# Performance work log

Hardware: AMD Instinct MI355X
Metric: run time of the kernel (lower is better)

Reference implementation:

```python
import jax, jax.numpy as jnp
import numpy as np

D = 1024
H = 16
DH = D // H  # 64
EPS = 1e-5


def _ln(x, w, b=None):
    mu = jnp.mean(x, axis=-1, keepdims=True)
    var = jnp.var(x, axis=-1, keepdims=True)
    y = (x - mu) * jax.lax.rsqrt(var + EPS) * w
    return y + b if b is not None else y


def _rotate_half(x):
    x1, x2 = jnp.split(x, 2, axis=-1)
    return jnp.concatenate([-x2, x1], axis=-1)


def _rope(q, k):
    # q, k: [B, L, H, DH]; rotary over sequence dim (ESM-style half-split rotation)
    L = q.shape[1]
    inv_freq = 1.0 / (10000.0 ** (jnp.arange(0, DH, 2, dtype=jnp.float32) / DH))
    freqs = jnp.arange(L, dtype=jnp.float32)[:, None] * inv_freq[None, :]  # [L, DH/2]
    emb = jnp.concatenate([freqs, freqs], axis=-1)  # [L, DH]
    cos = jnp.cos(emb)[None, :, None, :]  # [1, L, 1, DH]
    sin = jnp.sin(emb)[None, :, None, :]
    q = q * cos + _rotate_half(q) * sin
    k = k * cos + _rotate_half(k) * sin
    return q, k


def setup_inputs() -> dict:
    key = jax.random.key(0)
    ks = jax.random.split(key, 8)
    B, L = 2, 2048
    x = jax.random.normal(ks[0], (B, L, D), dtype=jnp.float32)
    seq_id = jnp.sort(jax.random.randint(ks[1], (B, L), 0, 8), axis=-1)
    s = 1.0 / np.sqrt(D)
    return {
        "x": x,
        "seq_id": seq_id,
        "ln1_w": jnp.ones((D,), jnp.float32),
        "ln1_b": jnp.zeros((D,), jnp.float32),
        "w_qkv": jax.random.normal(ks[2], (3 * D, D), dtype=jnp.float32) * s,
        "q_ln_w": jnp.ones((D,), jnp.float32),
        "k_ln_w": jnp.ones((D,), jnp.float32),
        "out_w": jax.random.normal(ks[3], (D, D), dtype=jnp.float32) * s,
    }


def reference(x, seq_id, ln1_w, ln1_b, w_qkv, q_ln_w, k_ln_w, out_w):
    B, L, _ = x.shape
    h = _ln(x, ln1_w, ln1_b)
    qkv = jnp.einsum("bld,ed->ble", h, w_qkv)  # [B, L, 3D]
    q, k, v = jnp.split(qkv, 3, axis=-1)
    q = _ln(q, q_ln_w)
    k = _ln(k, k_ln_w)
    q = q.reshape(B, L, H, DH)
    k = k.reshape(B, L, H, DH)
    q, k = _rope(q, k)
    q = q.transpose(0, 2, 1, 3)  # [B, H, L, DH]
    k = k.transpose(0, 2, 1, 3)
    v = v.reshape(B, L, H, DH).transpose(0, 2, 1, 3)
    scale = 1.0 / np.sqrt(DH)
    scores = jnp.einsum("bhld,bhmd->bhlm", q, k) * scale  # [B, H, L, L]
    mask = (seq_id[:, None, :, None] == seq_id[:, None, None, :])  # [B, 1, L, L]
    scores = jnp.where(mask, scores, -jnp.inf)
    attn = jax.nn.softmax(scores, axis=-1)
    ctx = jnp.einsum("bhlm,bhmd->bhld", attn, v)  # [B, H, L, DH]
    ctx = ctx.transpose(0, 2, 1, 3).reshape(B, L, D)
    return jnp.einsum("bld,ed->ble", ctx, out_w)
```

## Files before the change

kernel.cpp:

```cpp
#include <hip/hip_runtime.h>
#include <hip/hip_bf16.h>
#include <math.h>

#define D 1024
#define H 16
#define DH 64
#define L 2048
#define B 2
#define NROW (B * L)
#define EPS 1e-5f

typedef _Float16 half8 __attribute__((ext_vector_type(8)));
typedef _Float16 half4v __attribute__((ext_vector_type(4)));
typedef float f32x4 __attribute__((ext_vector_type(4)));

__global__ __launch_bounds__(256) void prep_kernel(const float* __restrict__ x,
                                                   const float* __restrict__ lw,
                                                   const float* __restrict__ lb,
                                                   _Float16* __restrict__ h16,
                                                   const float* __restrict__ wqkv,
                                                   _Float16* __restrict__ wqkv16,
                                                   const float* __restrict__ outw,
                                                   _Float16* __restrict__ outw16,
                                                   const int* __restrict__ seq_id,
                                                   int* __restrict__ lo,
                                                   int* __restrict__ hi,
                                                   float2* __restrict__ rtab) {
    int blk = blockIdx.x;
    int t = threadIdx.x;
    if (blk < 4096) {
        int r = blk;
        const float* xr = x + (size_t)r * D;
        float4 v = *(const float4*)&xr[t * 4];
        float s = v.x + v.y + v.z + v.w;
        float sq = v.x * v.x + v.y * v.y + v.z * v.z + v.w * v.w;
        for (int off = 32; off > 0; off >>= 1) {
            s += __shfl_xor(s, off, 64);
            sq += __shfl_xor(sq, off, 64);
        }
        __shared__ float ls[4], lq[4];
        int wave = t >> 6;
        if ((t & 63) == 0) { ls[wave] = s; lq[wave] = sq; }
        __syncthreads();
        float S = ls[0] + ls[1] + ls[2] + ls[3];
        float Q = lq[0] + lq[1] + lq[2] + lq[3];
        float mu = S / (float)D;
        float rs = rsqrtf(Q / (float)D - mu * mu + EPS);
        float4 w4 = *(const float4*)&lw[t * 4];
        float4 b4 = *(const float4*)&lb[t * 4];
        half4v o = {(_Float16)((v.x - mu) * rs * w4.x + b4.x),
                    (_Float16)((v.y - mu) * rs * w4.y + b4.y),
                    (_Float16)((v.z - mu) * rs * w4.z + b4.z),
                    (_Float16)((v.w - mu) * rs * w4.w + b4.w)};
        *(half4v*)&h16[(size_t)r * D + t * 4] = o;
    } else if (blk < 6144) {
        int base = blk - 4096;
        const float* src;
        _Float16* dst;
        if (base < 1536) { src = wqkv; dst = wqkv16; }
        else             { src = outw; dst = outw16; base -= 1536; }
        int i = (base * 256 + t) * 8;
        float4 a = *(const float4*)&src[i];
        float4 b = *(const float4*)&src[i + 4];
        half8 h = {(_Float16)a.x, (_Float16)a.y, (_Float16)a.z, (_Float16)a.w,
                   (_Float16)b.x, (_Float16)b.y, (_Float16)b.z, (_Float16)b.w};
        *(half8*)&dst[i] = h;
    } else if (blk < 6160) {
        int idx = (blk - 6144) * 256 + t;
        int b = idx / L, l = idx - b * L;
        const int* row = seq_id + (size_t)b * L;
        int v = row[l];
        int a = 0, c = L;
        while (a < c) { int m = (a + c) >> 1; if (row[m] < v) a = m + 1; else c = m; }
        lo[idx] = a;
        a = 0; c = L;
        while (a < c) { int m = (a + c) >> 1; if (row[m] <= v) a = m + 1; else c = m; }
        hi[idx] = a;
    } else {
        int idx = (blk - 6160) * 256 + t;
        int l = idx >> 5, fi = idx & 31;
        float invf = expf(-(float)fi * 0.28782313662425572f);
        float sn, cs;
        sincosf((float)l * invf, &sn, &cs);
        rtab[idx] = make_float2(cs, sn);
    }
}

template <typename OutT, int BM, int BN, bool VSPLIT>
__global__ __launch_bounds__(256) void gemm_f16_kernel(const _Float16* __restrict__ A,
                                                       const _Float16* __restrict__ W,
                                                       OutT* __restrict__ C, int N,
                                                       _Float16* __restrict__ v_t) {
    constexpr int WM = BM / 2, WN = BN / 2;
    constexpr int MT = WM / 16, NT = WN / 16;
    __shared__ _Float16 As[2][BM * 32];
    __shared__ _Float16 Bs[2][BN * 32];
    int t = threadIdx.x;
    int w = t >> 6, lane = t & 63;
    int quad = lane >> 4, col = lane & 15;
    int nx = gridDim.x;
    int ib = blockIdx.y * nx + blockIdx.x;
    int nwg = nx * gridDim.y;
    int ni = (ib & 7) * (nwg >> 3) + (ib >> 3);
    int m0 = (ni / nx) * BM, n0 = (ni % nx) * BN;
    int mw = (w >> 1) * WM, nw = (w & 1) * WN;
    int sw = (col >> 1) & 3;

    f32x4 acc[MT][NT] = {};

    auto stage = [&](int k0, int buf) {
#pragma unroll
        for (int i = 0; i < BM / 64; i++) {
            int e = t + i * 256;
            int row = e >> 2, kc = (e & 3) ^ ((row >> 1) & 3);
            __builtin_amdgcn_global_load_lds(
                (const __attribute__((address_space(1))) void*)&A[(size_t)(m0 + row) * 1024 + k0 + kc * 8],
                (__attribute__((address_space(3))) void*)&As[buf][e * 8], 16, 0, 0);
        }
#pragma unroll
        for (int i = 0; i < BN / 64; i++) {
            int e = t + i * 256;
            int row = e >> 2, kc = (e & 3) ^ ((row >> 1) & 3);
            __builtin_amdgcn_global_load_lds(
                (const __attribute__((address_space(1))) void*)&W[(size_t)(n0 + row) * 1024 + k0 + kc * 8],
                (__attribute__((address_space(3))) void*)&Bs[buf][e * 8], 16, 0, 0);
        }
    };

    stage(0, 0);
    int cur = 0;
    for (int k0 = 0; k0 < 1024; k0 += 32) {
        __syncthreads();
        if (k0 + 32 < 1024) stage(k0 + 32, cur ^ 1);
        half8 af[MT], bf[NT];
#pragma unroll
        for (int mt = 0; mt < MT; mt++)
            af[mt] = *(const half8*)&As[cur][(mw + mt * 16 + col) * 32 + ((quad ^ sw) << 3)];
#pragma unroll
        for (int nt = 0; nt < NT; nt++)
            bf[nt] = *(const half8*)&Bs[cur][(nw + nt * 16 + col) * 32 + ((quad ^ sw) << 3)];
#pragma unroll
        for (int mt = 0; mt < MT; mt++)
#pragma unroll
            for (int nt = 0; nt < NT; nt++)
                acc[mt][nt] = __builtin_amdgcn_mfma_f32_16x16x32_f16(af[mt], bf[nt], acc[mt][nt], 0, 0, 0);
        cur ^= 1;
    }

    if (VSPLIT && n0 >= 2048) {
        int b = m0 >> 11;
#pragma unroll
        for (int mt = 0; mt < MT; mt++)
#pragma unroll
            for (int nt = 0; nt < NT; nt++) {
                int vcol = n0 - 2048 + nw + nt * 16 + col;
                int bh = b * H + (vcol >> 6);
                int d = vcol & 63;
                int l = (m0 & (L - 1)) + mw + mt * 16 + quad * 4;
                half4v pk = {(_Float16)acc[mt][nt][0], (_Float16)acc[mt][nt][1],
                             (_Float16)acc[mt][nt][2], (_Float16)acc[mt][nt][3]};
                *(half4v*)&v_t[((size_t)(bh * 64 + d)) * 2048 + l] = pk;
            }
    } else {
#pragma unroll
        for (int mt = 0; mt < MT; mt++)
#pragma unroll
            for (int nt = 0; nt < NT; nt++)
#pragma unroll
                for (int r = 0; r < 4; r++) {
                    int row = m0 + mw + mt * 16 + quad * 4 + r;
                    int cc = n0 + nw + nt * 16 + col;
                    C[(size_t)row * N + cc] = (OutT)acc[mt][nt][r];
                }
    }
}

__global__ __launch_bounds__(256) void mid_kernel(const _Float16* __restrict__ qkv,
                                                  const float* __restrict__ qw,
                                                  const float* __restrict__ kw,
                                                  const float2* __restrict__ rtab,
                                                  _Float16* __restrict__ q_r,
                                                  _Float16* __restrict__ k_r) {
    __shared__ float ls[4], lq[4];
    int t = threadIdx.x;
    int r = blockIdx.x;
    int half = t >> 7;
    int tt = t & 127;
    const _Float16* src = qkv + (size_t)r * 3072 + half * 1024;
    const float* wgt = half ? kw : qw;
    _Float16* dst = half ? k_r : q_r;

    half8 hv = *(const half8*)&src[tt * 8];
    float y[8];
    float s = 0.f, sq = 0.f;
#pragma unroll
    for (int e = 0; e < 8; e++) {
        float v = (float)hv[e];
        y[e] = v;
        s += v;
        sq += v * v;
    }
    for (int off = 32; off > 0; off >>= 1) {
        s += __shfl_xor(s, off, 64);
        sq += __shfl_xor(sq, off, 64);
    }
    int wave = t >> 6;
    if ((t & 63) == 0) { ls[wave] = s; lq[wave] = sq; }
    __syncthreads();
    int base = half << 1;
    float S = ls[base] + ls[base + 1];
    float Q = lq[base] + lq[base + 1];
    float mu = S / 1024.f;
    float rs = rsqrtf(Q / 1024.f - mu * mu + EPS);

    int l = r & (L - 1);
    int b = r >> 11;
    int j0 = tt * 8;
    int dh0 = j0 & 63, hh = j0 >> 6;
    const float2* cp = &rtab[l * 32 + (dh0 & 31)];
    float4 c01 = *(const float4*)cp;
    float4 c23 = *(const float4*)(cp + 2);
    float4 c45 = *(const float4*)(cp + 4);
    float4 c67 = *(const float4*)(cp + 6);
    float cs_[8] = {c01.x, c01.z, c23.x, c23.z, c45.x, c45.z, c67.x, c67.z};
    float sn_[8] = {c01.y, c01.w, c23.y, c23.w, c45.y, c45.w, c67.y, c67.w};

    float yn[8];
#pragma unroll
    for (int e = 0; e < 8; e++) yn[e] = (y[e] - mu) * rs * wgt[j0 + e];
    float sgn = (dh0 < 32) ? -1.f : 1.f;
    half8 o;
#pragma unroll
    for (int e = 0; e < 8; e++) {
        float p = __shfl_xor(yn[e], 4, 64);
        o[e] = (_Float16)(yn[e] * cs_[e] + sgn * p * sn_[e]);
    }
    *(half8*)&dst[((size_t)((b * H + hh) * L + l)) * 64 + dh0] = o;
}

__global__ __launch_bounds__(512) void attn_mfma_kernel(const _Float16* __restrict__ q_r,
                                                        const _Float16* __restrict__ k_r,
                                                        const _Float16* __restrict__ v_t,
                                                        const int* __restrict__ lo_arr,
                                                        const int* __restrict__ hi_arr,
                                                        _Float16* __restrict__ ctx) {
    __shared__ _Float16 Ks[2][64][64];
    __shared__ _Float16 Vs[2][64][64];
    __shared__ _Float16 Ps[8][16][64];
    int bh = blockIdx.y;
    int b = bh >> 4, h = bh & 15;
    int l0 = blockIdx.x * 128;
    int t = threadIdx.x;
    int w = t >> 6, lane = t & 63;
    int quad = lane >> 4, col = lane & 15;
    int rbase = l0 + w * 16;

    int blo = lo_arr[b * L + l0] & ~63;
    int bhi = hi_arr[b * L + l0 + 127];

    auto stage = [&](int m0, int buf) {
        int row = t >> 3, ch = t & 7;
        int sch = ch ^ (row & 7);
        __builtin_amdgcn_global_load_lds(
            (const __attribute__((address_space(1))) void*)&k_r[((size_t)(bh * L + m0 + row)) * 64 + sch * 8],
            (__attribute__((address_space(3))) void*)&Ks[buf][row][ch * 8], 16, 0, 0);
        __builtin_amdgcn_global_load_lds(
            (const __attribute__((address_space(1))) void*)&v_t[((size_t)(bh * 64 + row)) * 2048 + m0 + sch * 8],
            (__attribute__((address_space(3))) void*)&Vs[buf][row][ch * 8], 16, 0, 0);
    };

    stage(blo, 0);

    half8 qf0, qf1;
    {
        const _Float16* qp = q_r + ((size_t)(bh * L + rbase + col)) * 64 + quad * 8;
        qf0 = *(const half8*)qp;
        qf1 = *(const half8*)(qp + 32);
    }
    int lo_c = lo_arr[b * L + rbase + col];
    int hi_c = hi_arr[b * L + rbase + col];
    int wlo = __shfl(lo_c, 15, 64);
    int whi = __shfl(hi_c, 0, 64);

    f32x4 o[4] = {};
    float m_run = -1e30f, l_run = 0.f;
    const float SCL = 0.125f * 1.4426950408889634f;
    int swz = (col & 7) << 3;
    int src = (lane & 48) | ((lane & 48) >> 2);

    int cur = 0;
    for (int m0 = blo; m0 < bhi; m0 += 64) {
        __syncthreads();
        if (m0 + 64 < bhi) stage(m0 + 64, cur ^ 1);

        f32x4 s[4] = {};
#pragma unroll
        for (int nt = 0; nt < 4; nt++) {
            int key = nt * 16 + col;
            const _Float16* kp = &Ks[cur][key][0];
            half8 kf0 = *(const half8*)&kp[(quad ^ (key & 7)) * 8];
            half8 kf1 = *(const half8*)&kp[((quad + 4) ^ (key & 7)) * 8];
            s[nt] = __builtin_amdgcn_mfma_f32_16x16x32_f16(kf0, qf0, s[nt], 0, 0, 0);
            s[nt] = __builtin_amdgcn_mfma_f32_16x16x32_f16(kf1, qf1, s[nt], 0, 0, 0);
        }

        float p[4][4];
        bool full = (m0 >= wlo) && (m0 + 64 <= whi);
        if (full) {
#pragma unroll
            for (int nt = 0; nt < 4; nt++)
#pragma unroll
                for (int r = 0; r < 4; r++) p[nt][r] = s[nt][r] * SCL;
        } else {
#pragma unroll
            for (int nt = 0; nt < 4; nt++) {
                int kb = m0 + nt * 16 + quad * 4;
#pragma unroll
                for (int r = 0; r < 4; r++) {
                    int key = kb + r;
                    p[nt][r] = (key >= lo_c && key < hi_c) ? s[nt][r] * SCL : -INFINITY;
                }
            }
        }

        float tmax = p[0][0];
#pragma unroll
        for (int nt = 0; nt < 4; nt++)
#pragma unroll
            for (int r = 0; r < 4; r++) tmax = fmaxf(tmax, p[nt][r]);
        tmax = fmaxf(tmax, __shfl_xor(tmax, 16, 64));
        tmax = fmaxf(tmax, __shfl_xor(tmax, 32, 64));
        float nm = fmaxf(m_run, tmax);
        float corr = exp2f(m_run - nm);
        m_run = nm;
        float rs = 0.f;
#pragma unroll
        for (int nt = 0; nt < 4; nt++)
#pragma unroll
            for (int r = 0; r < 4; r++) {
                float e2 = exp2f(p[nt][r] - nm);
                p[nt][r] = e2;
                rs += e2;
            }
        rs += __shfl_xor(rs, 16, 64);
        rs += __shfl_xor(rs, 32, 64);
        l_run = l_run * corr + rs;

#pragma unroll
        for (int nt = 0; nt < 4; nt++) {
            half4v pk = {(_Float16)p[nt][0], (_Float16)p[nt][1],
                         (_Float16)p[nt][2], (_Float16)p[nt][3]};
            *(half4v*)&Ps[w][col][(nt * 16 + quad * 4) ^ swz] = pk;
        }

#pragma unroll
        for (int r = 0; r < 4; r++) {
            float c4 = __shfl(corr, src + r, 64);
            o[0][r] *= c4; o[1][r] *= c4; o[2][r] *= c4; o[3][r] *= c4;
        }

        half8 pf0 = *(const half8*)&Ps[w][col][(quad * 8) ^ swz];
        half8 pf1 = *(const half8*)&Ps[w][col][(32 + quad * 8) ^ swz];
#pragma unroll
        for (int nt = 0; nt < 4; nt++) {
            int dr = nt * 16 + col;
            const _Float16* vp = &Vs[cur][dr][0];
            half8 vf0 = *(const half8*)&vp[(quad ^ (dr & 7)) * 8];
            half8 vf1 = *(const half8*)&vp[((quad + 4) ^ (dr & 7)) * 8];
            o[nt] = __builtin_amdgcn_mfma_f32_16x16x32_f16(pf0, vf0, o[nt], 0, 0, 0);
            o[nt] = __builtin_amdgcn_mfma_f32_16x16x32_f16(pf1, vf1, o[nt], 0, 0, 0);
        }
        cur ^= 1;
    }

#pragma unroll
    for (int r = 0; r < 4; r++) {
        float linv = 1.f / __shfl(l_run, src + r, 64);
        int row = rbase + quad * 4 + r;
#pragma unroll
        for (int nt = 0; nt < 4; nt++)
            ctx[((size_t)(b * L + row)) * 1024 + h * 64 + nt * 16 + col] =
                (_Float16)(o[nt][r] * linv);
    }
}

extern "C" void kernel_launch(void* const* d_in, const int* in_sizes, int n_in,
                              void* d_out, int out_size, void* d_ws, size_t ws_size,
                              hipStream_t stream) {
    const float* x      = (const float*)d_in[0];
    const int*   seq_id = (const int*)d_in[1];
    const float* ln1_w  = (const float*)d_in[2];
    const float* ln1_b  = (const float*)d_in[3];
    const float* w_qkv  = (const float*)d_in[4];
    const float* q_ln_w = (const float*)d_in[5];
    const float* k_ln_w = (const float*)d_in[6];
    const float* out_w  = (const float*)d_in[7];
    float* out = (float*)d_out;

    char* ws = (char*)d_ws;
    int*      lo     = (int*)(ws);
    int*      hi     = (int*)(ws + (64 << 10));
    float2*   rtab   = (float2*)(ws + (128 << 10));
    _Float16* h16    = (_Float16*)(ws + (1ull << 20));
    _Float16* wqkv16 = (_Float16*)(ws + (10ull << 20));
    _Float16* outw16 = (_Float16*)(ws + (17ull << 20));
    _Float16* qkv16  = (_Float16*)(ws + (20ull << 20));
    _Float16* q_r    = (_Float16*)(ws + (45ull << 20));
    _Float16* k_r    = (_Float16*)(ws + (54ull << 20));
    _Float16* v_t    = (_Float16*)(ws + (63ull << 20));
    _Float16* ctx16  = (_Float16*)(ws + (72ull << 20));

    prep_kernel<<<dim3(6416), dim3(256), 0, stream>>>(
        x, ln1_w, ln1_b, h16, w_qkv, wqkv16, out_w, outw16, seq_id, lo, hi, rtab);
    gemm_f16_kernel<_Float16, 128, 128, true><<<dim3(3072 / 128, NROW / 128), dim3(256), 0, stream>>>(
        h16, wqkv16, qkv16, 3072, v_t);
    mid_kernel<<<dim3(4096), dim3(256), 0, stream>>>(qkv16, q_ln_w, k_ln_w, rtab, q_r, k_r);
    attn_mfma_kernel<<<dim3(L / 128, B * H), dim3(512), 0, stream>>>(q_r, k_r, v_t, lo, hi, ctx16);
    gemm_f16_kernel<float, 128, 64, false><<<dim3(1024 / 64, NROW / 128), dim3(256), 0, stream>>>(
        ctx16, outw16, out, 1024, nullptr);

    (void)in_sizes; (void)n_in; (void)out_size; (void)ws_size;
}
```

Measured before the change: 186.0 us.

## Replace QKV GEMM with 256x256 eight-phase pipelined kernel using direct-to-LDS loads

Adds a dedicated QKV projection kernel with 256x256 tiles, 512 threads and a K-step of 64. It loads global data straight into XOR-swizzled LDS with global_load_lds. Each K iteration is split into four load/MMA phases with barriers and setprio, so the next tile's loads overlap with MFMA work. A CU-aware tile remap covers 192 blocks. The goal is higher MFMA utilization and operand reuse in the largest GEMM. The costs are more register pressure, more barriers, and a grid smaller than the CU count, which can leave some CUs idle.

```diff
diff --git a/kernel.cpp b/kernel.cpp
--- a/kernel.cpp
+++ b/kernel.cpp
@@ -86,11 +86,140 @@
     }
 }
 
-template <typename OutT, int BM, int BN, bool VSPLIT>
+#define LDA_HALF(BUF, MH, DST)                                                      \
+    _Pragma("unroll") for (int mt = 0; mt < 4; mt++) {                              \
+        int row_ = mw + (MH) * 64 + mt * 16 + col;                                  \
+        _Pragma("unroll") for (int kk = 0; kk < 2; kk++)                            \
+            DST[mt][kk] = *(const half8*)&As[BUF][row_][((kk * 4 + quad) ^ (row_ & 7)) * 8]; \
+    }
+
+#define LDB_HALF(BUF, NH, DST)                                                      \
+    _Pragma("unroll") for (int nt = 0; nt < 2; nt++) {                              \
+        int row_ = nw + (NH) * 32 + nt * 16 + col;                                  \
+        _Pragma("unroll") for (int kk = 0; kk < 2; kk++)                            \
+            DST[nt][kk] = *(const half8*)&Bs[BUF][row_][((kk * 4 + quad) ^ (row_ & 7)) * 8]; \
+    }
+
+#define MMA_QUAD(MH, NH, AF, BF)                                                    \
+    __builtin_amdgcn_s_setprio(1);                                                  \
+    _Pragma("unroll") for (int mt = 0; mt < 4; mt++)                                \
+    _Pragma("unroll") for (int nt = 0; nt < 2; nt++) {                              \
+        acc[(MH) * 4 + mt][(NH) * 2 + nt] = __builtin_amdgcn_mfma_f32_16x16x32_f16( \
+            AF[mt][0], BF[nt][0], acc[(MH) * 4 + mt][(NH) * 2 + nt], 0, 0, 0);      \
+        acc[(MH) * 4 + mt][(NH) * 2 + nt] = __builtin_amdgcn_mfma_f32_16x16x32_f16( \
+            AF[mt][1], BF[nt][1], acc[(MH) * 4 + mt][(NH) * 2 + nt], 0, 0, 0);      \
+    }                                                                               \
+    __builtin_amdgcn_s_setprio(0);
+
+__global__ __launch_bounds__(512, 2) void gemm1_8phase(const _Float16* __restrict__ A,
+                                                       const _Float16* __restrict__ W,
+                                                       _Float16* __restrict__ C,
+                                                       _Float16* __restrict__ v_t) {
+    __shared__ _Float16 As[2][256][64];
+    __shared__ _Float16 Bs[2][256][64];
+    int t = threadIdx.x;
+    int w = t >> 6, lane = t & 63;
+    int quad = lane >> 4, col = lane & 15;
+
+    int i = blockIdx.y * 12 + blockIdx.x;
+    int xcd = i & 7, j = i >> 3;
+    int tm = (xcd >> 1) * 4 + j / 6;
+    int tn = (xcd & 1) * 6 + j % 6;
+    int m0 = tm * 256, n0 = tn * 256;
+    int mw = (w >> 2) * 128, nw = (w & 3) * 64;
+
+    f32x4 acc[8][4] = {};
+
+    auto stageA = [&](int kt, int buf, int half) {
+#pragma unroll
+        for (int ii = 0; ii < 2; ii++) {
+            int e = half * 1024 + ii * 512 + t;
+            int row = e >> 3, ch = e & 7;
+            int sch = ch ^ (row & 7);
+            __builtin_amdgcn_global_load_lds(
+                (const __attribute__((address_space(1))) void*)&A[(size_t)(m0 + row) * 1024 + kt * 64 + sch * 8],
+                (__attribute__((address_space(3))) void*)&As[buf][row][ch * 8], 16, 0, 0);
+        }
+    };
+    auto stageB = [&](int kt, int buf, int half) {
+#pragma unroll
+        for (int ii = 0; ii < 2; ii++) {
+            int e = half * 1024 + ii * 512 + t;
+            int row = e >> 3, ch = e & 7;
+            int sch = ch ^ (row & 7);
+            __builtin_amdgcn_global_load_lds(
+                (const __attribute__((address_space(1))) void*)&W[(size_t)(n0 + row) * 1024 + kt * 64 + sch * 8],
+                (__attribute__((address_space(3))) void*)&Bs[buf][row][ch * 8], 16, 0, 0);
+        }
+    };
+
+    stageA(0, 0, 0); stageA(0, 0, 1); stageB(0, 0, 0); stageB(0, 0, 1);
+    stageA(1, 1, 0);
+    asm volatile("s_waitcnt vmcnt(2)" ::: "memory");
+    __builtin_amdgcn_s_barrier();
+
+    half8 af[4][2], bf0[2][2], bf1[2][2];
+    for (int kt = 0; kt < 16; kt++) {
+        int p = kt & 1, np = p ^ 1;
+
+        LDA_HALF(p, 0, af);
+        LDB_HALF(p, 0, bf0);
+        if (kt + 1 < 16) stageA(kt + 1, np, 1);
+        __builtin_amdgcn_s_barrier();
+        MMA_QUAD(0, 0, af, bf0);
+        __builtin_amdgcn_s_barrier();
+
+        LDB_HALF(p, 1, bf1);
+        if (kt + 1 < 16) stageB(kt + 1, np, 0);
+        __builtin_amdgcn_s_barrier();
+        MMA_QUAD(0, 1, af, bf1);
+        __builtin_amdgcn_s_barrier();
+
+        LDA_HALF(p, 1, af);
+        if (kt + 1 < 16) stageB(kt + 1, np, 1);
+        __builtin_amdgcn_s_barrier();
+        MMA_QUAD(1, 1, af, bf1);
+        __builtin_amdgcn_s_barrier();
+
+        if (kt + 2 < 16) stageA(kt + 2, p, 0);
+        MMA_QUAD(1, 0, af, bf0);
+        if (kt < 14)       { asm volatile("s_waitcnt vmcnt(2)" ::: "memory"); }
+        else if (kt == 14) { asm volatile("s_waitcnt vmcnt(0)" ::: "memory"); }
+        if (kt < 15) __builtin_amdgcn_s_barrier();
+    }
+
+    if (n0 >= 2048) {
+        int b = m0 >> 11;
+#pragma unroll
+        for (int mt = 0; mt < 8; mt++)
+#pragma unroll
+            for (int nt = 0; nt < 4; nt++) {
+                int vcol = n0 - 2048 + nw + nt * 16 + col;
+                int bh = b * H + (vcol >> 6);
+                int d = vcol & 63;
+                int l = (m0 & (L - 1)) + mw + mt * 16 + quad * 4;
+                half4v pk = {(_Float16)acc[mt][nt][0], (_Float16)acc[mt][nt][1],
+                             (_Float16)acc[mt][nt][2], (_Float16)acc[mt][nt][3]};
+                *(half4v*)&v_t[((size_t)(bh * 64 + d)) * 2048 + l] = pk;
+            }
+    } else {
+#pragma unroll
+        for (int mt = 0; mt < 8; mt++)
+#pragma unroll
+            for (int nt = 0; nt < 4; nt++)
+#pragma unroll
+                for (int r = 0; r < 4; r++) {
+                    int row = m0 + mw + mt * 16 + quad * 4 + r;
+                    int cc = n0 + nw + nt * 16 + col;
+                    C[(size_t)row * 3072 + cc] = (_Float16)acc[mt][nt][r];
+                }
+    }
+}
+
+template <typename OutT, int BM, int BN>
 __global__ __launch_bounds__(256) void gemm_f16_kernel(const _Float16* __restrict__ A,
                                                        const _Float16* __restrict__ W,
-                                                       OutT* __restrict__ C, int N,
-                                                       _Float16* __restrict__ v_t) {
+                                                       OutT* __restrict__ C, int N) {
     constexpr int WM = BM / 2, WN = BN / 2;
     constexpr int MT = WM / 16, NT = WN / 16;
     __shared__ _Float16 As[2][BM * 32];
@@ -147,32 +276,16 @@
         cur ^= 1;
     }
 
-    if (VSPLIT && n0 >= 2048) {
-        int b = m0 >> 11;
-#pragma unroll
-        for (int mt = 0; mt < MT; mt++)
-#pragma unroll
-            for (int nt = 0; nt < NT; nt++) {
-                int vcol = n0 - 2048 + nw + nt * 16 + col;
-                int bh = b * H + (vcol >> 6);
-                int d = vcol & 63;
-                int l = (m0 & (L - 1)) + mw + mt * 16 + quad * 4;
-                half4v pk = {(_Float16)acc[mt][nt][0], (_Float16)acc[mt][nt][1],
-                             (_Float16)acc[mt][nt][2], (_Float16)acc[mt][nt][3]};
-                *(half4v*)&v_t[((size_t)(bh * 64 + d)) * 2048 + l] = pk;
+#pragma unroll
+    for (int mt = 0; mt < MT; mt++)
+#pragma unroll
+        for (int nt = 0; nt < NT; nt++)
+#pragma unroll
+            for (int r = 0; r < 4; r++) {
+                int row = m0 + mw + mt * 16 + quad * 4 + r;
+                int cc = n0 + nw + nt * 16 + col;
+                C[(size_t)row * N + cc] = (OutT)acc[mt][nt][r];
             }
-    } else {
-#pragma unroll
-        for (int mt = 0; mt < MT; mt++)
-#pragma unroll
-            for (int nt = 0; nt < NT; nt++)
-#pragma unroll
-                for (int r = 0; r < 4; r++) {
-                    int row = m0 + mw + mt * 16 + quad * 4 + r;
-                    int cc = n0 + nw + nt * 16 + col;
-                    C[(size_t)row * N + cc] = (OutT)acc[mt][nt][r];
-                }
-    }
 }
 
 __global__ __launch_bounds__(256) void mid_kernel(const _Float16* __restrict__ qkv,
@@ -412,12 +525,11 @@
 
     prep_kernel<<<dim3(6416), dim3(256), 0, stream>>>(
         x, ln1_w, ln1_b, h16, w_qkv, wqkv16, out_w, outw16, seq_id, lo, hi, rtab);
-    gemm_f16_kernel<_Float16, 128, 128, true><<<dim3(3072 / 128, NROW / 128), dim3(256), 0, stream>>>(
-        h16, wqkv16, qkv16, 3072, v_t);
+    gemm1_8phase<<<dim3(12, 16), dim3(512), 0, stream>>>(h16, wqkv16, qkv16, v_t);
     mid_kernel<<<dim3(4096), dim3(256), 0, stream>>>(qkv16, q_ln_w, k_ln_w, rtab, q_r, k_r);
     attn_mfma_kernel<<<dim3(L / 128, B * H), dim3(512), 0, stream>>>(q_r, k_r, v_t, lo, hi, ctx16);
-    gemm_f16_kernel<float, 128, 64, false><<<dim3(1024 / 64, NROW / 128), dim3(256), 0, stream>>>(
-        ctx16, outw16, out, 1024, nullptr);
+    gemm_f16_kernel<float, 128, 64><<<dim3(1024 / 64, NROW / 128), dim3(256), 0, stream>>>(
+        ctx16, outw16, out, 1024);
 
     (void)in_sizes; (void)n_in; (void)out_size; (void)ws_size;
 }
```

After: 184.5 us. No clear change (-0.8%).
